# Kernel optimization log

Hardware: AMD Instinct MI355X
Metric: run time of the kernel (lower is better)

The kernel has to match this reference:

```python
import jax, jax.numpy as jnp
import numpy as np

T, A = 4096, 4          # tokens, atoms per token
N = T * A               # flat atoms
QB, KB = 32, 128        # query block / key window (AF3 atom transformer)
S = N // QB             # number of query subsets
H, DK = 4, 32           # heads, key dim per head
NB = 3                  # transformer blocks
CA, CP, CT = 128, 16, 384

# clipped sliding key window centered on each 32-atom query block
KIDX = jnp.clip(jnp.arange(S)[:, None] * QB - (KB - QB) // 2 + jnp.arange(KB)[None, :], 0, N - 1)

PARAM_SHAPES = [('w_ref_pos', (3, CA)), ('w_ref_mask', (1, CA)), ('w_ref_element', (CA, CA)), ('w_ref_charge', (1, CA)), ('w_ref_atom_name', (256, CA)), ('w_s2p_row', (CA, CP)), ('w_s2p_col', (CA, CP)), ('w_pair_offsets', (3, CP)), ('w_pair_dist', (1, CP)), ('w_pair_mask', (1, CP)), ('w_pair_mlp1', (CP, CP)), ('w_pair_mlp2', (CP, CP)), ('w_pair_mlp3', (CP, CP)), ('w_pair_ln', (CP,)), ('w_pair_logits', (CP, NB * H)), ('aq_lnw', (NB, CA)), ('aq_gw', (NB, CA, CA)), ('aq_gb', (NB, CA)), ('aq_sw', (NB, CA, CA)), ('ak_lnw', (NB, CA)), ('ak_gw', (NB, CA, CA)), ('ak_gb', (NB, CA)), ('ak_sw', (NB, CA, CA)), ('wq', (NB, CA, CA)), ('bq', (NB, CA)), ('wk', (NB, CA, CA)), ('wv', (NB, CA, CA)), ('wg', (NB, CA, CA)), ('azi_w', (NB, CA, CA)), ('azi_cw', (NB, CA, CA)), ('azi_cb', (NB, CA)), ('t_lnw', (NB, CA)), ('t_gw', (NB, CA, CA)), ('t_gb', (NB, CA)), ('t_sw', (NB, CA, CA)), ('glu1', (NB, CA, 2 * CA)), ('glu2', (NB, CA, 2 * CA)), ('t_azi_w', (NB, 2 * CA, CA)), ('t_azi_cw', (NB, CA, CA)), ('t_azi_cb', (NB, CA)), ('w_project', (CA, CT))]


def _ln(x, w=None, eps=1e-5):
    mu = jnp.mean(x, -1, keepdims=True)
    var = jnp.var(x, -1, keepdims=True)
    xn = (x - mu) * jax.lax.rsqrt(var + eps)
    return xn * w if w is not None else xn


def _ada_ln(x, cond, lnw, gw, gb, sw):
    c = _ln(cond, lnw)
    return jax.nn.sigmoid(c @ gw + gb) * _ln(x) + c @ sw


def setup_inputs() -> dict:
    ks = iter(jax.random.split(jax.random.key(0), 64))
    d = {}
    d['positions'] = jax.random.normal(next(ks), (T, A, 3), jnp.float32) * 3.0
    d['mask'] = jnp.ones((T, A), jnp.float32)
    d['element'] = jax.random.randint(next(ks), (T, A), 0, 128, jnp.int32)
    d['charge'] = jax.random.normal(next(ks), (T, A), jnp.float32)
    d['atom_name_chars'] = jax.random.randint(next(ks), (T, A, 4), 0, 64, jnp.int32)
    d['ref_space_uid'] = jax.random.randint(next(ks), (T, A), 0, T, jnp.int32)
    for nm, shp in PARAM_SHAPES:
        if nm.endswith('lnw') or nm == 'w_pair_ln':
            d[nm] = jnp.ones(shp, jnp.float32)
        else:
            d[nm] = jax.random.normal(next(ks), shp, jnp.float32) * 0.02
    return d


def _forward(positions, mask, charge, w_ref_pos, w_ref_mask, w_ref_element, w_ref_charge, w_ref_atom_name, w_s2p_row, w_s2p_col, w_pair_offsets, w_pair_dist, w_pair_mask, w_pair_mlp1, w_pair_mlp2, w_pair_mlp3, w_pair_ln, w_pair_logits, aq_lnw, aq_gw, aq_gb, aq_sw, ak_lnw, ak_gw, ak_gb, ak_sw, wq, bq, wk, wv, wg, azi_w, azi_cw, azi_cb, t_lnw, t_gw, t_gb, t_sw, glu1, glu2, t_azi_w, t_azi_cw, t_azi_cb, w_project, element, atom_name_chars, ref_space_uid):
    dt = positions.dtype
    pos = positions.reshape(N, 3)
    m = mask.reshape(N, 1)
    # per_atom_cond
    el1h = jax.nn.one_hot(element.reshape(N), 128, dtype=dt)
    nm1h = jax.nn.one_hot(atom_name_chars.reshape(N, 4), 64, dtype=dt).reshape(N, 256)
    ch = jnp.arcsinh(charge.reshape(N, 1))
    act = pos @ w_ref_pos + m @ w_ref_mask + el1h @ w_ref_element + ch @ w_ref_charge + nm1h @ w_ref_atom_name
    act = act * m
    qsc = act.reshape(S, QB, CA)  # queries_single_cond
    # pair conditioning
    uid = ref_space_uid.reshape(N)
    q_uid, k_uid = uid.reshape(S, QB), uid[KIDX]
    q_pos, k_pos = pos.reshape(S, QB, 3), pos[KIDX]
    valid = (q_uid[:, :, None] == k_uid[:, None, :]).astype(dt)[..., None]  # [S,QB,KB,1]
    off = q_pos[:, :, None, :] - k_pos[:, None, :, :]  # [S,QB,KB,3]
    pair = (off @ w_pair_offsets) * valid
    sq = jnp.sum(off * off, -1, keepdims=True)
    pair = pair + ((1.0 / (1.0 + sq)) @ w_pair_dist) * valid
    ksc = act[KIDX]  # keys_single_cond [S,KB,CA]
    pair = pair + (jax.nn.relu(qsc) @ w_s2p_row)[:, :, None, :] + (jax.nn.relu(ksc) @ w_s2p_col)[:, None, :, :]
    pair = pair + valid @ w_pair_mask
    t = jax.nn.relu(pair) @ w_pair_mlp1
    t = jax.nn.relu(t) @ w_pair_mlp2
    t = jax.nn.relu(t) @ w_pair_mlp3
    pair = pair + t
    # pair logits for all blocks: [NB, S, H, QB, KB]
    pl = (_ln(pair, w_pair_ln) @ w_pair_logits).reshape(S, QB, KB, NB, H)
    pl = jnp.transpose(pl, (3, 0, 4, 1, 2))
    qact = qsc
    scale = DK ** -0.5
    for i in range(NB):
        kact = qact.reshape(N, CA)[KIDX]
        xq = _ada_ln(qact, qsc, aq_lnw[i], aq_gw[i], aq_gb[i], aq_sw[i])
        xk = _ada_ln(kact, ksc, ak_lnw[i], ak_gw[i], ak_gb[i], ak_sw[i])
        q = (xq @ wq[i] + bq[i]).reshape(S, QB, H, DK)
        k = (xk @ wk[i]).reshape(S, KB, H, DK)
        logits = jnp.einsum('sqhd,skhd->shqk', q * scale, k) + pl[i]
        aw = jax.nn.softmax(logits, axis=-1)
        v = (xk @ wv[i]).reshape(S, KB, H, DK)
        o = jnp.einsum('shqk,skhd->sqhd', aw, v).reshape(S, QB, CA)
        o = o * jax.nn.sigmoid(xq @ wg[i])
        o = (o @ azi_w[i]) * jax.nn.sigmoid(qsc @ azi_cw[i] + azi_cb[i])  # AdaptiveZeroInit
        qact = qact + o
        xt = _ada_ln(qact, qsc, t_lnw[i], t_gw[i], t_gb[i], t_sw[i])
        xt = jax.nn.silu(xt @ glu1[i]) * (xt @ glu2[i])  # SwiGLU
        xt = (xt @ t_azi_w[i]) * jax.nn.sigmoid(qsc @ t_azi_cw[i] + t_azi_cb[i])
        qact = qact + xt
    tok = jax.nn.relu(qact.reshape(T, A, CA) @ w_project)
    mm = mask[..., None]
    token_act = jnp.sum(tok * mm, -2) / jnp.maximum(jnp.sum(mm, -2), 1e-10)
    return token_act, qact, qsc, pair


def reference(positions, mask, element, charge, atom_name_chars, ref_space_uid, w_ref_pos, w_ref_mask, w_ref_element, w_ref_charge, w_ref_atom_name, w_s2p_row, w_s2p_col, w_pair_offsets, w_pair_dist, w_pair_mask, w_pair_mlp1, w_pair_mlp2, w_pair_mlp3, w_pair_ln, w_pair_logits, aq_lnw, aq_gw, aq_gb, aq_sw, ak_lnw, ak_gw, ak_gb, ak_sw, wq, bq, wk, wv, wg, azi_w, azi_cw, azi_cb, t_lnw, t_gw, t_gb, t_sw, glu1, glu2, t_azi_w, t_azi_cw, t_azi_cb, w_project):
    return _forward(positions, mask, charge, w_ref_pos, w_ref_mask, w_ref_element, w_ref_charge, w_ref_atom_name, w_s2p_row, w_s2p_col, w_pair_offsets, w_pair_dist, w_pair_mask, w_pair_mlp1, w_pair_mlp2, w_pair_mlp3, w_pair_ln, w_pair_logits, aq_lnw, aq_gw, aq_gb, aq_sw, ak_lnw, ak_gw, ak_gb, ak_sw, wq, bq, wk, wv, wg, azi_w, azi_cw, azi_cb, t_lnw, t_gw, t_gb, t_sw, glu1, glu2, t_azi_w, t_azi_cw, t_azi_cb, w_project, element, atom_name_chars, ref_space_uid)
```

## Files before the change

kernel.cpp:

```cpp
#include <hip/hip_runtime.h>
#include <math.h>

#define TT 4096
#define AA 4
#define NN 16384
#define QBQ 32
#define KBK 128
#define SS 512
#define HH 4
#define DKD 32
#define CAC 128
#define CPC 16
#define CTC 384

#define EPI_PLAIN 0
#define EPI_SIG   1
#define EPI_RELU  3

typedef __attribute__((ext_vector_type(8))) short bf16x8;
typedef __attribute__((ext_vector_type(4))) short s16x4;
typedef __attribute__((ext_vector_type(4))) float f32x4;

__device__ __forceinline__ float sig_(float x) { return 1.0f / (1.0f + __expf(-x)); }
__device__ __forceinline__ short f2bf(float f) {
    unsigned u = __float_as_uint(f);
    unsigned r = (u + 0x7FFFu + ((u >> 16) & 1u)) >> 16;
    return (short)r;
}
__device__ __forceinline__ float b2f(short s) {
    return __uint_as_float(((unsigned)(unsigned short)s) << 16);
}

struct PEnt { const float* src; const float* rs; short* dst; int K; int NC; };
struct PTab { PEnt e[49]; };

__global__ __launch_bounds__(256) void k_prep(PTab tab)
{
    const PEnt e = tab.e[blockIdx.y];
    const int ntx = e.NC >> 5, nty = e.K >> 5, nt = ntx * nty;
    __shared__ float sm[32][33];
    const int lx = threadIdx.x & 31, ly = threadIdx.x >> 5;
    for (int t = blockIdx.x; t < nt; t += gridDim.x) {
        const int ty = t / ntx, tx = t - ty * ntx;
        #pragma unroll
        for (int j = 0; j < 4; ++j) {
            const int k = ty * 32 + ly + j * 8;
            const int n = tx * 32 + lx;
            float v = e.src[(size_t)k * e.NC + n];
            if (e.rs) v *= e.rs[k];
            sm[ly + j * 8][lx] = v;
        }
        __syncthreads();
        #pragma unroll
        for (int j = 0; j < 4; ++j) {
            const int n = tx * 32 + ly + j * 8;
            const int k = ty * 32 + lx;
            e.dst[(size_t)n * e.K + k] = f2bf(sm[lx][ly + j * 8]);
        }
        __syncthreads();
    }
}

__global__ __launch_bounds__(128) void k_atom_cond(
    const float* __restrict__ pos, const float* __restrict__ msk,
    const int* __restrict__ elem, const float* __restrict__ chg,
    const int* __restrict__ chars,
    const float* __restrict__ w_pos, const float* __restrict__ w_msk,
    const float* __restrict__ w_elem, const float* __restrict__ w_chg,
    const float* __restrict__ w_name,
    const float* __restrict__ w_row, const float* __restrict__ w_col,
    float* __restrict__ qsc, float* __restrict__ qact,
    short* __restrict__ qsc_bf, short* __restrict__ qn_bf,
    float* __restrict__ rq, float* __restrict__ rk)
{
    const int n = blockIdx.x, c = threadIdx.x;
    const float p0 = pos[n*3+0], p1 = pos[n*3+1], p2 = pos[n*3+2];
    const float m = msk[n];
    const int   el = elem[n];
    const float ach = asinhf(chg[n]);
    const int c0 = chars[n*4+0], c1 = chars[n*4+1], c2 = chars[n*4+2], c3 = chars[n*4+3];

    float a = p0*w_pos[c] + p1*w_pos[CAC+c] + p2*w_pos[2*CAC+c]
            + m*w_msk[c] + w_elem[el*CAC+c] + ach*w_chg[c]
            + w_name[(c0      )*CAC+c] + w_name[( 64+c1)*CAC+c]
            + w_name[(128+c2)*CAC+c] + w_name[(192+c3)*CAC+c];
    a *= m;

    const size_t base = (size_t)n*CAC + c;
    qsc[base] = a; qact[base] = a; qsc_bf[base] = f2bf(a);

    __shared__ float red[128];
    __shared__ float sh[128];
    red[c] = a; __syncthreads();
    for (int off = 64; off > 0; off >>= 1) { if (c < off) red[c] += red[c+off]; __syncthreads(); }
    const float mu = red[0] * (1.0f/128.0f);
    __syncthreads();
    const float d = a - mu;
    red[c] = d*d; __syncthreads();
    for (int off = 64; off > 0; off >>= 1) { if (c < off) red[c] += red[c+off]; __syncthreads(); }
    const float var = red[0] * (1.0f/128.0f);
    qn_bf[base] = f2bf(d * rsqrtf(var + 1e-5f));
    __syncthreads();
    sh[c] = fmaxf(a, 0.0f);
    __syncthreads();
    if (c < 32) {
        const float* w = (c < 16) ? w_row : w_col;
        const int cc = c & 15;
        float acc = 0.0f;
        #pragma unroll 8
        for (int r = 0; r < 128; ++r) acc += sh[r] * w[r*CPC + cc];
        if (c < 16) rq[(size_t)n*CPC + cc] = acc;
        else        rk[(size_t)n*CPC + cc] = acc;
    }
}

__global__ __launch_bounds__(256) void k_pair(
    const float* __restrict__ pos, const int* __restrict__ uid,
    const float* __restrict__ rq, const float* __restrict__ rk,
    const float* __restrict__ w_ofs, const float* __restrict__ w_dist,
    const float* __restrict__ w_pm,
    const float* __restrict__ mlp1, const float* __restrict__ mlp2,
    const float* __restrict__ mlp3,
    const float* __restrict__ wln, const float* __restrict__ wpl,
    float* __restrict__ pair, short* __restrict__ plb)
{
    __shared__ float sm1[256], sm2[256], sm3[256], sofs[48], sdist[16], smask[16];
    __shared__ float swln[16], swpl[192];
    const int tid = threadIdx.x;
    sm1[tid] = mlp1[tid]; sm2[tid] = mlp2[tid]; sm3[tid] = mlp3[tid];
    if (tid < 48) sofs[tid] = w_ofs[tid];
    if (tid < 16) { sdist[tid] = w_dist[tid]; smask[tid] = w_pm[tid]; swln[tid] = wln[tid]; }
    if (tid < 192) swpl[tid] = wpl[tid];
    __syncthreads();

    const int gid = blockIdx.x*256 + tid;
    const int s = gid >> 12;
    const int rem = gid & 4095;
    const int q = rem >> 7, kk = rem & 127;
    const int n = s*QBQ + q;
    int kidx = s*QBQ - 48 + kk; kidx = max(0, min(NN-1, kidx));

    const float v = (uid[n] == uid[kidx]) ? 1.0f : 0.0f;
    const float o0 = pos[n*3+0]-pos[kidx*3+0];
    const float o1 = pos[n*3+1]-pos[kidx*3+1];
    const float o2 = pos[n*3+2]-pos[kidx*3+2];
    const float sq = o0*o0 + o1*o1 + o2*o2;
    const float inv = 1.0f/(1.0f + sq);

    const float* rqp = rq + (size_t)n*CPC;
    const float* rkp = rk + (size_t)kidx*CPC;

    float p[16], t1[16], t2[16];
    #pragma unroll
    for (int j = 0; j < 16; ++j)
        p[j] = v*(o0*sofs[j] + o1*sofs[16+j] + o2*sofs[32+j] + inv*sdist[j] + smask[j])
             + rqp[j] + rkp[j];
    #pragma unroll
    for (int j = 0; j < 16; ++j) {
        float acc = 0.0f;
        #pragma unroll
        for (int r = 0; r < 16; ++r) acc += fmaxf(p[r], 0.0f) * sm1[r*16+j];
        t1[j] = acc;
    }
    #pragma unroll
    for (int j = 0; j < 16; ++j) {
        float acc = 0.0f;
        #pragma unroll
        for (int r = 0; r < 16; ++r) acc += fmaxf(t1[r], 0.0f) * sm2[r*16+j];
        t2[j] = acc;
    }
    #pragma unroll
    for (int j = 0; j < 16; ++j) {
        float acc = 0.0f;
        #pragma unroll
        for (int r = 0; r < 16; ++r) acc += fmaxf(t2[r], 0.0f) * sm3[r*16+j];
        t1[j] = p[j] + acc;
    }
    float* op = pair + (size_t)gid*CPC;
    #pragma unroll
    for (int j = 0; j < 4; ++j)
        *(float4*)(op + j*4) = make_float4(t1[j*4], t1[j*4+1], t1[j*4+2], t1[j*4+3]);

    float sm = 0.0f;
    #pragma unroll
    for (int j = 0; j < 16; ++j) sm += t1[j];
    const float mu = sm * (1.0f/16.0f);
    float vq = 0.0f;
    #pragma unroll
    for (int j = 0; j < 16; ++j) { const float dd = t1[j]-mu; vq += dd*dd; }
    const float rs = rsqrtf(vq*(1.0f/16.0f) + 1e-5f);
    float xn[16];
    #pragma unroll
    for (int j = 0; j < 16; ++j) xn[j] = (t1[j]-mu)*rs*swln[j];
    #pragma unroll
    for (int i = 0; i < 3; ++i) {
        #pragma unroll
        for (int h = 0; h < 4; ++h) {
            float acc = 0.0f;
            #pragma unroll
            for (int j = 0; j < 16; ++j) acc += xn[j] * swpl[j*12 + i*4 + h];
            plb[((((size_t)i*SS + s)*HH + h)*QBQ + q)*KBK + kk] = f2bf(acc);
        }
    }
}

__global__ __launch_bounds__(128) void k_rowln(const float* __restrict__ x, float* __restrict__ y)
{
    const int n = blockIdx.x, c = threadIdx.x;
    __shared__ float red[128];
    const float v = x[(size_t)n*CAC + c];
    red[c] = v; __syncthreads();
    for (int off = 64; off > 0; off >>= 1) { if (c < off) red[c] += red[c+off]; __syncthreads(); }
    const float mu = red[0] * (1.0f/128.0f);
    __syncthreads();
    const float d = v - mu;
    red[c] = d*d; __syncthreads();
    for (int off = 64; off > 0; off >>= 1) { if (c < off) red[c] += red[c+off]; __syncthreads(); }
    const float var = red[0] * (1.0f/128.0f);
    y[(size_t)n*CAC + c] = d * rsqrtf(var + 1e-5f);
}

struct MJob {
    const short* A; const short* Bt; const float* bias;
    float* outF; short* outB;
    int K; int ostride; int epi;
};
struct MJobs { MJob j[8]; };

__global__ __launch_bounds__(256) void k_mm(MJobs jobs)
{
    __shared__ short As[128*64];
    __shared__ short Bs[128*64];
    const MJob J = jobs.j[blockIdx.y];
    const int tid = threadIdx.x;
    const int wave = tid >> 6, lane = tid & 63;
    const int l15 = lane & 15, l4 = lane >> 4;
    const int row0 = blockIdx.x * 128;
    const int K = J.K;

    f32x4 acc[2][8];
    #pragma unroll
    for (int m = 0; m < 2; ++m)
        #pragma unroll
        for (int n = 0; n < 8; ++n) acc[m][n] = (f32x4){0.f,0.f,0.f,0.f};

    for (int k0 = 0; k0 < K; k0 += 64) {
        #pragma unroll
        for (int j = 0; j < 4; ++j) {
            const int u = tid + j*256;
            const int r = u >> 3, ug = u & 7;
            const bf16x8 av = *(const bf16x8*)(J.A + (size_t)(row0 + r)*K + k0 + ug*8);
            *(bf16x8*)&As[r*64 + ((ug ^ (r & 7)) * 8)] = av;
            const bf16x8 bv = *(const bf16x8*)(J.Bt + (size_t)r*K + k0 + ug*8);
            *(bf16x8*)&Bs[r*64 + ((ug ^ (r & 7)) * 8)] = bv;
        }
        __syncthreads();
        #pragma unroll
        for (int ks = 0; ks < 2; ++ks) {
            bf16x8 af[2], bfr[8];
            #pragma unroll
            for (int m = 0; m < 2; ++m) {
                const int r = wave*32 + m*16 + l15;
                af[m] = *(const bf16x8*)&As[r*64 + (((ks*4 + l4) ^ (r & 7)) * 8)];
            }
            #pragma unroll
            for (int n = 0; n < 8; ++n) {
                const int c = n*16 + l15;
                bfr[n] = *(const bf16x8*)&Bs[c*64 + (((ks*4 + l4) ^ (c & 7)) * 8)];
            }
            #pragma unroll
            for (int m = 0; m < 2; ++m)
                #pragma unroll
                for (int n = 0; n < 8; ++n)
                    acc[m][n] = __builtin_amdgcn_mfma_f32_16x16x32_bf16(af[m], bfr[n], acc[m][n], 0, 0, 0);
        }
        __syncthreads();
    }

    float bval[8];
    #pragma unroll
    for (int n = 0; n < 8; ++n) bval[n] = 0.0f;
    if (J.bias) {
        #pragma unroll
        for (int n = 0; n < 8; ++n) bval[n] = J.bias[n*16 + l15];
    }
    const int epi = J.epi;
    #pragma unroll
    for (int m = 0; m < 2; ++m) {
        #pragma unroll
        for (int n = 0; n < 8; ++n) {
            const int col = n*16 + l15;
            #pragma unroll
            for (int reg = 0; reg < 4; ++reg) {
                const int row = row0 + wave*32 + m*16 + l4*4 + reg;
                float v = acc[m][n][reg] + bval[n];
                if (epi == EPI_SIG)  v = sig_(v);
                if (epi == EPI_RELU) v = fmaxf(v, 0.0f);
                if (J.outB) J.outB[(size_t)row*J.ostride + col] = f2bf(v);
                else        J.outF[(size_t)row*J.ostride + col] = v;
            }
        }
    }
}

__global__ __launch_bounds__(512) void k_attn2(
    const float* __restrict__ qh, const float* __restrict__ kh,
    const float* __restrict__ vh, const short* __restrict__ pls,
    float* __restrict__ oh)
{
    __shared__ float sm_m[256], sm_l[256], sm_acc[256*17];
    const int s = blockIdx.x, tid = threadIdx.x;
    const int kh2 = tid >> 8;
    const int h = (tid >> 6) & 3;
    const int q = (tid >> 1) & 31;
    const int dh = tid & 1;
    const int n0 = s*QBQ;
    const int kbase = n0 - 48 + kh2*64;
    const float SCALE = 0.17677669529663687f;

    float qr[32];
    {
        const float* qp = qh + (size_t)(n0+q)*CAC + h*DKD;
        #pragma unroll
        for (int j = 0; j < 8; ++j) {
            const float4 v4 = *(const float4*)(qp + j*4);
            qr[j*4]=v4.x*SCALE; qr[j*4+1]=v4.y*SCALE; qr[j*4+2]=v4.z*SCALE; qr[j*4+3]=v4.w*SCALE;
        }
    }
    const short* plp = pls + (((size_t)s*HH + h)*QBQ + q)*KBK + kh2*64;

    float m = -1e30f, l = 0.0f;
    float acc[16];
    #pragma unroll
    for (int j = 0; j < 16; ++j) acc[j] = 0.0f;

    for (int kb4 = 0; kb4 < 16; ++kb4) {
        const s16x4 p4 = *(const s16x4*)(plp + kb4*4);
        float pv[4];
        #pragma unroll
        for (int j = 0; j < 4; ++j) pv[j] = b2f(p4[j]);
        #pragma unroll
        for (int j = 0; j < 4; ++j) {
            const int kb = kb4*4 + j;
            int kidx = kbase + kb; kidx = max(0, min(NN-1, kidx));
            const float* kp = kh + (size_t)kidx*CAC + h*DKD;
            float dot = 0.0f;
            #pragma unroll
            for (int jj = 0; jj < 8; ++jj) {
                const float4 kv = *(const float4*)(kp + jj*4);
                dot += qr[jj*4]*kv.x + qr[jj*4+1]*kv.y + qr[jj*4+2]*kv.z + qr[jj*4+3]*kv.w;
            }
            const float sv = dot + pv[j];
            if (sv > m) {
                const float corr = __expf(m - sv);
                l *= corr;
                #pragma unroll
                for (int d = 0; d < 16; ++d) acc[d] *= corr;
                m = sv;
            }
            const float w = __expf(sv - m);
            l += w;
            const float* vp = vh + (size_t)kidx*CAC + h*DKD + dh*16;
            #pragma unroll
            for (int jj = 0; jj < 4; ++jj) {
                const float4 vv = *(const float4*)(vp + jj*4);
                acc[jj*4]   = fmaf(w, vv.x, acc[jj*4]);
                acc[jj*4+1] = fmaf(w, vv.y, acc[jj*4+1]);
                acc[jj*4+2] = fmaf(w, vv.z, acc[jj*4+2]);
                acc[jj*4+3] = fmaf(w, vv.w, acc[jj*4+3]);
            }
        }
    }

    const int part = tid & 255;
    if (kh2 == 1) {
        sm_m[part] = m; sm_l[part] = l;
        #pragma unroll
        for (int j = 0; j < 16; ++j) sm_acc[part*17 + j] = acc[j];
    }
    __syncthreads();
    if (kh2 == 0) {
        const float m2 = sm_m[part], l2 = sm_l[part];
        const float mm = fmaxf(m, m2);
        const float c1 = __expf(m - mm), c2 = __expf(m2 - mm);
        const float inv = 1.0f / (l*c1 + l2*c2);
        float* op = oh + (size_t)(n0+q)*CAC + h*DKD + dh*16;
        #pragma unroll
        for (int jj = 0; jj < 4; ++jj) {
            float o0 = (acc[jj*4  ]*c1 + sm_acc[part*17+jj*4  ]*c2) * inv;
            float o1 = (acc[jj*4+1]*c1 + sm_acc[part*17+jj*4+1]*c2) * inv;
            float o2 = (acc[jj*4+2]*c1 + sm_acc[part*17+jj*4+2]*c2) * inv;
            float o3 = (acc[jj*4+3]*c1 + sm_acc[part*17+jj*4+3]*c2) * inv;
            *(float4*)op = make_float4(o0,o1,o2,o3);
            op += 4;
        }
    }
}

__global__ __launch_bounds__(256) void k_ada2(
    const float* __restrict__ qa,
    const short* __restrict__ G1, const short* __restrict__ S1,
    const short* __restrict__ G2, const short* __restrict__ S2,
    short* __restrict__ x1, short* __restrict__ x2)
{
    const int i = blockIdx.x*256 + threadIdx.x;
    const float4 a = ((const float4*)qa)[i];
    const s16x4 g1 = ((const s16x4*)G1)[i], s1 = ((const s16x4*)S1)[i];
    const s16x4 g2 = ((const s16x4*)G2)[i], s2 = ((const s16x4*)S2)[i];
    s16x4 o1, o2;
    o1[0] = f2bf(b2f(g1[0])*a.x + b2f(s1[0]));
    o1[1] = f2bf(b2f(g1[1])*a.y + b2f(s1[1]));
    o1[2] = f2bf(b2f(g1[2])*a.z + b2f(s1[2]));
    o1[3] = f2bf(b2f(g1[3])*a.w + b2f(s1[3]));
    o2[0] = f2bf(b2f(g2[0])*a.x + b2f(s2[0]));
    o2[1] = f2bf(b2f(g2[1])*a.y + b2f(s2[1]));
    o2[2] = f2bf(b2f(g2[2])*a.z + b2f(s2[2]));
    o2[3] = f2bf(b2f(g2[3])*a.w + b2f(s2[3]));
    ((s16x4*)x1)[i] = o1;
    ((s16x4*)x2)[i] = o2;
}

__global__ __launch_bounds__(256) void k_ada1(
    const float* __restrict__ qa,
    const short* __restrict__ G1, const short* __restrict__ S1,
    short* __restrict__ x1)
{
    const int i = blockIdx.x*256 + threadIdx.x;
    const float4 a = ((const float4*)qa)[i];
    const s16x4 g1 = ((const s16x4*)G1)[i], s1 = ((const s16x4*)S1)[i];
    s16x4 o1;
    o1[0] = f2bf(b2f(g1[0])*a.x + b2f(s1[0]));
    o1[1] = f2bf(b2f(g1[1])*a.y + b2f(s1[1]));
    o1[2] = f2bf(b2f(g1[2])*a.z + b2f(s1[2]));
    o1[3] = f2bf(b2f(g1[3])*a.w + b2f(s1[3]));
    ((s16x4*)x1)[i] = o1;
}

__global__ __launch_bounds__(256) void k_og(
    const float* __restrict__ o, const float* __restrict__ g, short* __restrict__ og)
{
    const int i = blockIdx.x*256 + threadIdx.x;
    const float4 a = ((const float4*)o)[i];
    const float4 b = ((const float4*)g)[i];
    s16x4 r;
    r[0] = f2bf(a.x*b.x); r[1] = f2bf(a.y*b.y); r[2] = f2bf(a.z*b.z); r[3] = f2bf(a.w*b.w);
    ((s16x4*)og)[i] = r;
}

__global__ __launch_bounds__(256) void k_axpy_g(
    float* __restrict__ y, const float* __restrict__ t,
    const short* __restrict__ g, short* __restrict__ ybf)
{
    const int i = blockIdx.x*256 + threadIdx.x;
    float4 yv = ((const float4*)y)[i];
    const float4 tv = ((const float4*)t)[i];
    const s16x4 gv = ((const s16x4*)g)[i];
    yv.x += tv.x * b2f(gv[0]);
    yv.y += tv.y * b2f(gv[1]);
    yv.z += tv.z * b2f(gv[2]);
    yv.w += tv.w * b2f(gv[3]);
    ((float4*)y)[i] = yv;
    if (ybf) {
        s16x4 r;
        r[0] = f2bf(yv.x); r[1] = f2bf(yv.y); r[2] = f2bf(yv.z); r[3] = f2bf(yv.w);
        ((s16x4*)ybf)[i] = r;
    }
}

__global__ __launch_bounds__(256) void k_silu_bf(
    const float* __restrict__ h1, const float* __restrict__ h2, short* __restrict__ hs)
{
    const int i = blockIdx.x*256 + threadIdx.x;
    const float4 a = ((const float4*)h1)[i];
    const float4 b = ((const float4*)h2)[i];
    s16x4 r;
    r[0] = f2bf(a.x * sig_(a.x) * b.x);
    r[1] = f2bf(a.y * sig_(a.y) * b.y);
    r[2] = f2bf(a.z * sig_(a.z) * b.z);
    r[3] = f2bf(a.w * sig_(a.w) * b.w);
    ((s16x4*)hs)[i] = r;
}

__global__ __launch_bounds__(256) void k_token_reduce(
    const float* __restrict__ tok, const float* __restrict__ msk, float* __restrict__ out)
{
    const int gid = blockIdx.x*256 + threadIdx.x;
    const int t = gid / CTC, c = gid - t*CTC;
    float num = 0.0f, den = 0.0f;
    #pragma unroll
    for (int a = 0; a < AA; ++a) {
        const float mv = msk[t*AA + a];
        num += tok[(size_t)(t*AA+a)*CTC + c] * mv;
        den += mv;
    }
    out[gid] = num / fmaxf(den, 1e-10f);
}

static inline MJob mj(const short* A, const short* Bt, const float* bias,
                      float* outF, short* outB, int K, int ostride, int epi)
{
    MJob j; j.A=A; j.Bt=Bt; j.bias=bias; j.outF=outF; j.outB=outB;
    j.K=K; j.ostride=ostride; j.epi=epi; return j;
}

extern "C" void kernel_launch(void* const* d_in, const int* in_sizes, int n_in,
                              void* d_out, int out_size, void* d_ws, size_t ws_size,
                              hipStream_t stream)
{
    const float* positions = (const float*)d_in[0];
    const float* maskp     = (const float*)d_in[1];
    const int*   element   = (const int*  )d_in[2];
    const float* charge    = (const float*)d_in[3];
    const int*   chars     = (const int*  )d_in[4];
    const int*   uid       = (const int*  )d_in[5];
    const float* w_ref_pos      = (const float*)d_in[6];
    const float* w_ref_mask     = (const float*)d_in[7];
    const float* w_ref_element  = (const float*)d_in[8];
    const float* w_ref_charge   = (const float*)d_in[9];
    const float* w_ref_atom_name= (const float*)d_in[10];
    const float* w_s2p_row      = (const float*)d_in[11];
    const float* w_s2p_col      = (const float*)d_in[12];
    const float* w_pair_offsets = (const float*)d_in[13];
    const float* w_pair_dist    = (const float*)d_in[14];
    const float* w_pair_mask    = (const float*)d_in[15];
    const float* w_pair_mlp1    = (const float*)d_in[16];
    const float* w_pair_mlp2    = (const float*)d_in[17];
    const float* w_pair_mlp3    = (const float*)d_in[18];
    const float* w_pair_ln      = (const float*)d_in[19];
    const float* w_pair_logits  = (const float*)d_in[20];
    const float* aq_lnw = (const float*)d_in[21];
    const float* aq_gw  = (const float*)d_in[22];
    const float* aq_gb  = (const float*)d_in[23];
    const float* aq_sw  = (const float*)d_in[24];
    const float* ak_lnw = (const float*)d_in[25];
    const float* ak_gw  = (const float*)d_in[26];
    const float* ak_gb  = (const float*)d_in[27];
    const float* ak_sw  = (const float*)d_in[28];
    const float* wq     = (const float*)d_in[29];
    const float* bq     = (const float*)d_in[30];
    const float* wk     = (const float*)d_in[31];
    const float* wv     = (const float*)d_in[32];
    const float* wg     = (const float*)d_in[33];
    const float* azi_w  = (const float*)d_in[34];
    const float* azi_cw = (const float*)d_in[35];
    const float* azi_cb = (const float*)d_in[36];
    const float* t_lnw  = (const float*)d_in[37];
    const float* t_gw   = (const float*)d_in[38];
    const float* t_gb   = (const float*)d_in[39];
    const float* t_sw   = (const float*)d_in[40];
    const float* glu1   = (const float*)d_in[41];
    const float* glu2   = (const float*)d_in[42];
    const float* t_azi_w  = (const float*)d_in[43];
    const float* t_azi_cw = (const float*)d_in[44];
    const float* t_azi_cb = (const float*)d_in[45];
    const float* w_project= (const float*)d_in[46];

    float* token_o = (float*)d_out;
    float* qact = token_o + 1572864;
    float* qsc  = token_o + 3670016;
    float* pair = token_o + 5767168;

    char* W = (char*)d_ws;
    short* pl_bf   = (short*)(W);
    short* wbf     = (short*)(W + 50331648);
    short* qn_bf   = (short*)(W + 52428800);
    short* qsc_bf  = (short*)(W + 56623104);
    float* qa      = (float*)(W + 60817408);
    short* Gq_bf   = (short*)(W + 69206016);
    short* Sq_bf   = (short*)(W + 73400320);
    short* Gk_bf   = (short*)(W + 77594624);
    short* Sk_bf   = (short*)(W + 81788928);
    short* Gt_bf   = (short*)(W + 85983232);
    short* St_bf   = (short*)(W + 90177536);
    short* Ag_bf   = (short*)(W + 94371840);
    short* Tg_bf   = (short*)(W + 98566144);
    short* xq_bf   = (short*)(W + 102760448);
    short* xk_bf   = (short*)(W + 106954752);
    float* w_q     = (float*)(W + 111149056);
    float* w_k     = (float*)(W + 119537664);
    float* w_v     = (float*)(W + 127926272);
    float* w_g     = (float*)(W + 136314880);
    float* w_o     = (float*)(W + 144703488);
    short* og_bf   = (short*)(W + 153092096);
    short* hs_bf   = (short*)(W + 157286400);
    short* qact_bf = (short*)(W + 165675008);
    float* rq      = (float*)(W + 169869312);
    float* rk      = (float*)(W + 174063616);
    float* h1  = w_q;
    float* h2  = w_v;
    float* tok = w_q;

    (void)in_sizes; (void)n_in; (void)out_size; (void)ws_size;

    const size_t LSTR = 311296;
    const size_t oGQ=0, oSQ=16384, oGK=32768, oSK=49152, oGT=65536, oST=81920,
                 oWQ=98304, oWK=114688, oWV=131072, oWG=147456, oAZ=163840,
                 oACW=180224, oTCW=196608, oG1=212992, oG2=245760, oTAW=278528;
    const size_t oPROJ = 3*LSTR;

    {
        PTab tab{};
        int e = 0;
        for (int i = 0; i < 3; ++i) {
            short* L = wbf + (size_t)i*LSTR;
            const size_t oM = (size_t)i*CAC*CAC, oV = (size_t)i*CAC, oGL = (size_t)i*CAC*2*CAC;
            tab.e[e++] = {aq_gw+oM,  aq_lnw+oV, L+oGQ,  128, 128};
            tab.e[e++] = {aq_sw+oM,  aq_lnw+oV, L+oSQ,  128, 128};
            tab.e[e++] = {ak_gw+oM,  ak_lnw+oV, L+oGK,  128, 128};
            tab.e[e++] = {ak_sw+oM,  ak_lnw+oV, L+oSK,  128, 128};
            tab.e[e++] = {t_gw+oM,   t_lnw+oV,  L+oGT,  128, 128};
            tab.e[e++] = {t_sw+oM,   t_lnw+oV,  L+oST,  128, 128};
            tab.e[e++] = {wq+oM,     nullptr,   L+oWQ,  128, 128};
            tab.e[e++] = {wk+oM,     nullptr,   L+oWK,  128, 128};
            tab.e[e++] = {wv+oM,     nullptr,   L+oWV,  128, 128};
            tab.e[e++] = {wg+oM,     nullptr,   L+oWG,  128, 128};
            tab.e[e++] = {azi_w+oM,  nullptr,   L+oAZ,  128, 128};
            tab.e[e++] = {azi_cw+oM, nullptr,   L+oACW, 128, 128};
            tab.e[e++] = {t_azi_cw+oM,nullptr,  L+oTCW, 128, 128};
            tab.e[e++] = {glu1+oGL,  nullptr,   L+oG1,  128, 256};
            tab.e[e++] = {glu2+oGL,  nullptr,   L+oG2,  128, 256};
            tab.e[e++] = {t_azi_w+oGL,nullptr,  L+oTAW, 256, 128};
        }
        tab.e[e++] = {w_project, nullptr, wbf+oPROJ, 128, 384};
        k_prep<<<dim3(48, 49), 256, 0, stream>>>(tab);
    }

    k_atom_cond<<<NN, 128, 0, stream>>>(positions, maskp, element, charge, chars,
        w_ref_pos, w_ref_mask, w_ref_element, w_ref_charge, w_ref_atom_name,
        w_s2p_row, w_s2p_col, qsc, qact, qsc_bf, qn_bf, rq, rk);

    k_pair<<<(SS*QBQ*KBK)/256, 256, 0, stream>>>(positions, uid, rq, rk,
        w_pair_offsets, w_pair_dist, w_pair_mask, w_pair_mlp1, w_pair_mlp2, w_pair_mlp3,
        w_pair_ln, w_pair_logits, pair, pl_bf);

    for (int i = 0; i < 3; ++i) {
        short* L = wbf + (size_t)i*LSTR;
        const size_t oV = (size_t)i*CAC;

        k_rowln<<<NN, 128, 0, stream>>>(qact, qa);

        {
            MJobs js{};
            js.j[0] = mj(qn_bf,  L+oGQ,  aq_gb+oV,    nullptr, Gq_bf, 128, 128, EPI_SIG);
            js.j[1] = mj(qn_bf,  L+oSQ,  nullptr,     nullptr, Sq_bf, 128, 128, EPI_PLAIN);
            js.j[2] = mj(qn_bf,  L+oGK,  ak_gb+oV,    nullptr, Gk_bf, 128, 128, EPI_SIG);
            js.j[3] = mj(qn_bf,  L+oSK,  nullptr,     nullptr, Sk_bf, 128, 128, EPI_PLAIN);
            js.j[4] = mj(qn_bf,  L+oGT,  t_gb+oV,     nullptr, Gt_bf, 128, 128, EPI_SIG);
            js.j[5] = mj(qn_bf,  L+oST,  nullptr,     nullptr, St_bf, 128, 128, EPI_PLAIN);
            js.j[6] = mj(qsc_bf, L+oACW, azi_cb+oV,   nullptr, Ag_bf, 128, 128, EPI_SIG);
            js.j[7] = mj(qsc_bf, L+oTCW, t_azi_cb+oV, nullptr, Tg_bf, 128, 128, EPI_SIG);
            k_mm<<<dim3(128, 8), 256, 0, stream>>>(js);
        }
        k_ada2<<<2048, 256, 0, stream>>>(qa, Gq_bf, Sq_bf, Gk_bf, Sk_bf, xq_bf, xk_bf);
        {
            MJobs js{};
            js.j[0] = mj(xq_bf, L+oWQ, bq+oV,   w_q, nullptr, 128, 128, EPI_PLAIN);
            js.j[1] = mj(xk_bf, L+oWK, nullptr, w_k, nullptr, 128, 128, EPI_PLAIN);
            js.j[2] = mj(xk_bf, L+oWV, nullptr, w_v, nullptr, 128, 128, EPI_PLAIN);
            js.j[3] = mj(xq_bf, L+oWG, nullptr, w_g, nullptr, 128, 128, EPI_SIG);
            k_mm<<<dim3(128, 4), 256, 0, stream>>>(js);
        }
        k_attn2<<<SS, 512, 0, stream>>>(w_q, w_k, w_v, pl_bf + (size_t)i*8388608, w_o);
        k_og<<<2048, 256, 0, stream>>>(w_o, w_g, og_bf);
        {
            MJobs js{};
            js.j[0] = mj(og_bf, L+oAZ, nullptr, w_o, nullptr, 128, 128, EPI_PLAIN);
            k_mm<<<dim3(128, 1), 256, 0, stream>>>(js);
        }
        k_axpy_g<<<2048, 256, 0, stream>>>(qact, w_o, Ag_bf, nullptr);
        k_rowln<<<NN, 128, 0, stream>>>(qact, qa);
        k_ada1<<<2048, 256, 0, stream>>>(qa, Gt_bf, St_bf, xq_bf);
        {
            MJobs js{};
            js.j[0] = mj(xq_bf, L+oG1,       nullptr, h1,     nullptr, 128, 256, EPI_PLAIN);
            js.j[1] = mj(xq_bf, L+oG1+16384, nullptr, h1+128, nullptr, 128, 256, EPI_PLAIN);
            js.j[2] = mj(xq_bf, L+oG2,       nullptr, h2,     nullptr, 128, 256, EPI_PLAIN);
            js.j[3] = mj(xq_bf, L+oG2+16384, nullptr, h2+128, nullptr, 128, 256, EPI_PLAIN);
            k_mm<<<dim3(128, 4), 256, 0, stream>>>(js);
        }
        k_silu_bf<<<4096, 256, 0, stream>>>(h1, h2, hs_bf);
        {
            MJobs js{};
            js.j[0] = mj(hs_bf, L+oTAW, nullptr, w_o, nullptr, 256, 128, EPI_PLAIN);
            k_mm<<<dim3(128, 1), 256, 0, stream>>>(js);
        }
        k_axpy_g<<<2048, 256, 0, stream>>>(qact, w_o, Tg_bf, (i == 2) ? qact_bf : nullptr);
    }

    {
        MJobs js{};
        js.j[0] = mj(qact_bf, wbf+oPROJ,       nullptr, tok,     nullptr, 128, 384, EPI_RELU);
        js.j[1] = mj(qact_bf, wbf+oPROJ+16384, nullptr, tok+128, nullptr, 128, 384, EPI_RELU);
        js.j[2] = mj(qact_bf, wbf+oPROJ+32768, nullptr, tok+256, nullptr, 128, 384, EPI_RELU);
        k_mm<<<dim3(128, 3), 256, 0, stream>>>(js);
    }
    k_token_reduce<<<(TT*CTC)/256, 256, 0, stream>>>(tok, maskp, token_o);
}
```

Before: 1.033 ms.

## Fuse residual, layernorm and adaLN; fold gating into GEMM A-load and SiLU-GLU epilogue

Merges the residual gated update, row layernorm and adaptive-LN modulation into a single per-row kernel, deferring the transition residual into the next block's first kernel with double-buffered gate buffers. The attention output gating is folded into the A-tile load of a dedicated GEMM, and the two GLU projections are computed in one GEMM with the SiLU-multiply in the epilogue. This removes several elementwise launches and the fp32 h1/h2 intermediates. The cost is more complex control flow and a GLU kernel that carries two accumulator sets.

```diff
diff --git a/kernel.cpp b/kernel.cpp
--- a/kernel.cpp
+++ b/kernel.cpp
@@ -204,20 +204,35 @@
     }
 }
 
-__global__ __launch_bounds__(128) void k_rowln(const float* __restrict__ x, float* __restrict__ y)
+__global__ __launch_bounds__(128) void k_resada(
+    float* __restrict__ qact, const float* __restrict__ o,
+    const short* __restrict__ g,
+    const short* __restrict__ G1, const short* __restrict__ S1,
+    const short* __restrict__ G2, const short* __restrict__ S2,
+    short* __restrict__ x1, short* __restrict__ x2, short* __restrict__ ybf)
 {
     const int n = blockIdx.x, c = threadIdx.x;
-    __shared__ float red[128];
-    const float v = x[(size_t)n*CAC + c];
-    red[c] = v; __syncthreads();
-    for (int off = 64; off > 0; off >>= 1) { if (c < off) red[c] += red[c+off]; __syncthreads(); }
-    const float mu = red[0] * (1.0f/128.0f);
-    __syncthreads();
-    const float d = v - mu;
-    red[c] = d*d; __syncthreads();
-    for (int off = 64; off > 0; off >>= 1) { if (c < off) red[c] += red[c+off]; __syncthreads(); }
-    const float var = red[0] * (1.0f/128.0f);
-    y[(size_t)n*CAC + c] = d * rsqrtf(var + 1e-5f);
+    const size_t base = (size_t)n*CAC + c;
+    float a = qact[base];
+    if (o) {
+        a += o[base] * b2f(g[base]);
+        qact[base] = a;
+    }
+    if (x1) {
+        __shared__ float red[128];
+        red[c] = a; __syncthreads();
+        for (int off = 64; off > 0; off >>= 1) { if (c < off) red[c] += red[c+off]; __syncthreads(); }
+        const float mu = red[0] * (1.0f/128.0f);
+        __syncthreads();
+        const float d = a - mu;
+        red[c] = d*d; __syncthreads();
+        for (int off = 64; off > 0; off >>= 1) { if (c < off) red[c] += red[c+off]; __syncthreads(); }
+        const float var = red[0] * (1.0f/128.0f);
+        const float ln = d * rsqrtf(var + 1e-5f);
+        x1[base] = f2bf(b2f(G1[base])*ln + b2f(S1[base]));
+        if (x2) x2[base] = f2bf(b2f(G2[base])*ln + b2f(S2[base]));
+    }
+    if (ybf) ybf[base] = f2bf(a);
 }
 
 struct MJob {
@@ -301,6 +316,156 @@
             }
         }
     }
+}
+
+__global__ __launch_bounds__(256) void k_mm_og(
+    const float* __restrict__ Ao, const float* __restrict__ Agt,
+    const short* __restrict__ Bt, float* __restrict__ out)
+{
+    __shared__ short As[128*64];
+    __shared__ short Bs[128*64];
+    const int tid = threadIdx.x;
+    const int wave = tid >> 6, lane = tid & 63;
+    const int l15 = lane & 15, l4 = lane >> 4;
+    const int row0 = blockIdx.x * 128;
+
+    f32x4 acc[2][8];
+    #pragma unroll
+    for (int m = 0; m < 2; ++m)
+        #pragma unroll
+        for (int n = 0; n < 8; ++n) acc[m][n] = (f32x4){0.f,0.f,0.f,0.f};
+
+    for (int k0 = 0; k0 < 128; k0 += 64) {
+        #pragma unroll
+        for (int j = 0; j < 4; ++j) {
+            const int u = tid + j*256;
+            const int r = u >> 3, ug = u & 7;
+            const size_t ab = (size_t)(row0 + r)*128 + k0 + ug*8;
+            const float4 oa = *(const float4*)(Ao + ab);
+            const float4 ob = *(const float4*)(Ao + ab + 4);
+            const float4 ga = *(const float4*)(Agt + ab);
+            const float4 gb = *(const float4*)(Agt + ab + 4);
+            bf16x8 av;
+            av[0]=f2bf(oa.x*ga.x); av[1]=f2bf(oa.y*ga.y); av[2]=f2bf(oa.z*ga.z); av[3]=f2bf(oa.w*ga.w);
+            av[4]=f2bf(ob.x*gb.x); av[5]=f2bf(ob.y*gb.y); av[6]=f2bf(ob.z*gb.z); av[7]=f2bf(ob.w*gb.w);
+            *(bf16x8*)&As[r*64 + ((ug ^ (r & 7)) * 8)] = av;
+            const bf16x8 bv = *(const bf16x8*)(Bt + (size_t)r*128 + k0 + ug*8);
+            *(bf16x8*)&Bs[r*64 + ((ug ^ (r & 7)) * 8)] = bv;
+        }
+        __syncthreads();
+        #pragma unroll
+        for (int ks = 0; ks < 2; ++ks) {
+            bf16x8 af[2], bfr[8];
+            #pragma unroll
+            for (int m = 0; m < 2; ++m) {
+                const int r = wave*32 + m*16 + l15;
+                af[m] = *(const bf16x8*)&As[r*64 + (((ks*4 + l4) ^ (r & 7)) * 8)];
+            }
+            #pragma unroll
+            for (int n = 0; n < 8; ++n) {
+                const int c = n*16 + l15;
+                bfr[n] = *(const bf16x8*)&Bs[c*64 + (((ks*4 + l4) ^ (c & 7)) * 8)];
+            }
+            #pragma unroll
+            for (int m = 0; m < 2; ++m)
+                #pragma unroll
+                for (int n = 0; n < 8; ++n)
+                    acc[m][n] = __builtin_amdgcn_mfma_f32_16x16x32_bf16(af[m], bfr[n], acc[m][n], 0, 0, 0);
+        }
+        __syncthreads();
+    }
+
+    #pragma unroll
+    for (int m = 0; m < 2; ++m)
+        #pragma unroll
+        for (int n = 0; n < 8; ++n) {
+            const int col = n*16 + l15;
+            #pragma unroll
+            for (int reg = 0; reg < 4; ++reg) {
+                const int row = row0 + wave*32 + m*16 + l4*4 + reg;
+                out[(size_t)row*128 + col] = acc[m][n][reg];
+            }
+        }
+}
+
+__global__ __launch_bounds__(256) void k_mm_glu(
+    const short* __restrict__ A, const short* __restrict__ B1t,
+    const short* __restrict__ B2t, short* __restrict__ out)
+{
+    __shared__ short As[128*64];
+    __shared__ short B1s[64*64];
+    __shared__ short B2s[64*64];
+    const int tid = threadIdx.x;
+    const int wave = tid >> 6, lane = tid & 63;
+    const int l15 = lane & 15, l4 = lane >> 4;
+    const int row0 = blockIdx.x * 128;
+    const int col0 = blockIdx.y * 64;
+
+    f32x4 acc1[2][4], acc2[2][4];
+    #pragma unroll
+    for (int m = 0; m < 2; ++m)
+        #pragma unroll
+        for (int n = 0; n < 4; ++n) {
+            acc1[m][n] = (f32x4){0.f,0.f,0.f,0.f};
+            acc2[m][n] = (f32x4){0.f,0.f,0.f,0.f};
+        }
+
+    for (int k0 = 0; k0 < 128; k0 += 64) {
+        #pragma unroll
+        for (int j = 0; j < 4; ++j) {
+            const int u = tid + j*256;
+            const int r = u >> 3, ug = u & 7;
+            const bf16x8 av = *(const bf16x8*)(A + (size_t)(row0 + r)*128 + k0 + ug*8);
+            *(bf16x8*)&As[r*64 + ((ug ^ (r & 7)) * 8)] = av;
+        }
+        #pragma unroll
+        for (int j = 0; j < 2; ++j) {
+            const int u = tid + j*256;
+            const int r = u >> 3, ug = u & 7;
+            const bf16x8 b1 = *(const bf16x8*)(B1t + (size_t)(col0 + r)*128 + k0 + ug*8);
+            *(bf16x8*)&B1s[r*64 + ((ug ^ (r & 7)) * 8)] = b1;
+            const bf16x8 b2 = *(const bf16x8*)(B2t + (size_t)(col0 + r)*128 + k0 + ug*8);
+            *(bf16x8*)&B2s[r*64 + ((ug ^ (r & 7)) * 8)] = b2;
+        }
+        __syncthreads();
+        #pragma unroll
+        for (int ks = 0; ks < 2; ++ks) {
+            bf16x8 af[2], bq1[4], bq2[4];
+            #pragma unroll
+            for (int m = 0; m < 2; ++m) {
+                const int r = wave*32 + m*16 + l15;
+                af[m] = *(const bf16x8*)&As[r*64 + (((ks*4 + l4) ^ (r & 7)) * 8)];
+            }
+            #pragma unroll
+            for (int n = 0; n < 4; ++n) {
+                const int c = n*16 + l15;
+                bq1[n] = *(const bf16x8*)&B1s[c*64 + (((ks*4 + l4) ^ (c & 7)) * 8)];
+                bq2[n] = *(const bf16x8*)&B2s[c*64 + (((ks*4 + l4) ^ (c & 7)) * 8)];
+            }
+            #pragma unroll
+            for (int m = 0; m < 2; ++m)
+                #pragma unroll
+                for (int n = 0; n < 4; ++n) {
+                    acc1[m][n] = __builtin_amdgcn_mfma_f32_16x16x32_bf16(af[m], bq1[n], acc1[m][n], 0, 0, 0);
+                    acc2[m][n] = __builtin_amdgcn_mfma_f32_16x16x32_bf16(af[m], bq2[n], acc2[m][n], 0, 0, 0);
+                }
+        }
+        __syncthreads();
+    }
+
+    #pragma unroll
+    for (int m = 0; m < 2; ++m)
+        #pragma unroll
+        for (int n = 0; n < 4; ++n) {
+            const int col = col0 + n*16 + l15;
+            #pragma unroll
+            for (int reg = 0; reg < 4; ++reg) {
+                const int row = row0 + wave*32 + m*16 + l4*4 + reg;
+                const float a1 = acc1[m][n][reg];
+                const float h = a1 * sig_(a1) * acc2[m][n][reg];
+                out[(size_t)row*256 + col] = f2bf(h);
+            }
+        }
 }
 
 __global__ __launch_bounds__(512) void k_attn2(
@@ -395,90 +560,6 @@
             op += 4;
         }
     }
-}
-
-__global__ __launch_bounds__(256) void k_ada2(
-    const float* __restrict__ qa,
-    const short* __restrict__ G1, const short* __restrict__ S1,
-    const short* __restrict__ G2, const short* __restrict__ S2,
-    short* __restrict__ x1, short* __restrict__ x2)
-{
-    const int i = blockIdx.x*256 + threadIdx.x;
-    const float4 a = ((const float4*)qa)[i];
-    const s16x4 g1 = ((const s16x4*)G1)[i], s1 = ((const s16x4*)S1)[i];
-    const s16x4 g2 = ((const s16x4*)G2)[i], s2 = ((const s16x4*)S2)[i];
-    s16x4 o1, o2;
-    o1[0] = f2bf(b2f(g1[0])*a.x + b2f(s1[0]));
-    o1[1] = f2bf(b2f(g1[1])*a.y + b2f(s1[1]));
-    o1[2] = f2bf(b2f(g1[2])*a.z + b2f(s1[2]));
-    o1[3] = f2bf(b2f(g1[3])*a.w + b2f(s1[3]));
-    o2[0] = f2bf(b2f(g2[0])*a.x + b2f(s2[0]));
-    o2[1] = f2bf(b2f(g2[1])*a.y + b2f(s2[1]));
-    o2[2] = f2bf(b2f(g2[2])*a.z + b2f(s2[2]));
-    o2[3] = f2bf(b2f(g2[3])*a.w + b2f(s2[3]));
-    ((s16x4*)x1)[i] = o1;
-    ((s16x4*)x2)[i] = o2;
-}
-
-__global__ __launch_bounds__(256) void k_ada1(
-    const float* __restrict__ qa,
-    const short* __restrict__ G1, const short* __restrict__ S1,
-    short* __restrict__ x1)
-{
-    const int i = blockIdx.x*256 + threadIdx.x;
-    const float4 a = ((const float4*)qa)[i];
-    const s16x4 g1 = ((const s16x4*)G1)[i], s1 = ((const s16x4*)S1)[i];
-    s16x4 o1;
-    o1[0] = f2bf(b2f(g1[0])*a.x + b2f(s1[0]));
-    o1[1] = f2bf(b2f(g1[1])*a.y + b2f(s1[1]));
-    o1[2] = f2bf(b2f(g1[2])*a.z + b2f(s1[2]));
-    o1[3] = f2bf(b2f(g1[3])*a.w + b2f(s1[3]));
-    ((s16x4*)x1)[i] = o1;
-}
-
-__global__ __launch_bounds__(256) void k_og(
-    const float* __restrict__ o, const float* __restrict__ g, short* __restrict__ og)
-{
-    const int i = blockIdx.x*256 + threadIdx.x;
-    const float4 a = ((const float4*)o)[i];
-    const float4 b = ((const float4*)g)[i];
-    s16x4 r;
-    r[0] = f2bf(a.x*b.x); r[1] = f2bf(a.y*b.y); r[2] = f2bf(a.z*b.z); r[3] = f2bf(a.w*b.w);
-    ((s16x4*)og)[i] = r;
-}
-
-__global__ __launch_bounds__(256) void k_axpy_g(
-    float* __restrict__ y, const float* __restrict__ t,
-    const short* __restrict__ g, short* __restrict__ ybf)
-{
-    const int i = blockIdx.x*256 + threadIdx.x;
-    float4 yv = ((const float4*)y)[i];
-    const float4 tv = ((const float4*)t)[i];
-    const s16x4 gv = ((const s16x4*)g)[i];
-    yv.x += tv.x * b2f(gv[0]);
-    yv.y += tv.y * b2f(gv[1]);
-    yv.z += tv.z * b2f(gv[2]);
-    yv.w += tv.w * b2f(gv[3]);
-    ((float4*)y)[i] = yv;
-    if (ybf) {
-        s16x4 r;
-        r[0] = f2bf(yv.x); r[1] = f2bf(yv.y); r[2] = f2bf(yv.z); r[3] = f2bf(yv.w);
-        ((s16x4*)ybf)[i] = r;
-    }
-}
-
-__global__ __launch_bounds__(256) void k_silu_bf(
-    const float* __restrict__ h1, const float* __restrict__ h2, short* __restrict__ hs)
-{
-    const int i = blockIdx.x*256 + threadIdx.x;
-    const float4 a = ((const float4*)h1)[i];
-    const float4 b = ((const float4*)h2)[i];
-    s16x4 r;
-    r[0] = f2bf(a.x * sig_(a.x) * b.x);
-    r[1] = f2bf(a.y * sig_(a.y) * b.y);
-    r[2] = f2bf(a.z * sig_(a.z) * b.z);
-    r[3] = f2bf(a.w * sig_(a.w) * b.w);
-    ((s16x4*)hs)[i] = r;
 }
 
 __global__ __launch_bounds__(256) void k_token_reduce(
@@ -565,7 +646,7 @@
     short* wbf     = (short*)(W + 50331648);
     short* qn_bf   = (short*)(W + 52428800);
     short* qsc_bf  = (short*)(W + 56623104);
-    float* qa      = (float*)(W + 60817408);
+    float* w_op    = (float*)(W + 60817408);
     short* Gq_bf   = (short*)(W + 69206016);
     short* Sq_bf   = (short*)(W + 73400320);
     short* Gk_bf   = (short*)(W + 77594624);
@@ -573,7 +654,7 @@
     short* Gt_bf   = (short*)(W + 85983232);
     short* St_bf   = (short*)(W + 90177536);
     short* Ag_bf   = (short*)(W + 94371840);
-    short* Tg_bf   = (short*)(W + 98566144);
+    short* Tg0_bf  = (short*)(W + 98566144);
     short* xq_bf   = (short*)(W + 102760448);
     short* xk_bf   = (short*)(W + 106954752);
     float* w_q     = (float*)(W + 111149056);
@@ -581,13 +662,11 @@
     float* w_v     = (float*)(W + 127926272);
     float* w_g     = (float*)(W + 136314880);
     float* w_o     = (float*)(W + 144703488);
-    short* og_bf   = (short*)(W + 153092096);
+    short* Tg1_bf  = (short*)(W + 153092096);
     short* hs_bf   = (short*)(W + 157286400);
     short* qact_bf = (short*)(W + 165675008);
     float* rq      = (float*)(W + 169869312);
     float* rk      = (float*)(W + 174063616);
-    float* h1  = w_q;
-    float* h2  = w_v;
     float* tok = w_q;
 
     (void)in_sizes; (void)n_in; (void)out_size; (void)ws_size;
@@ -636,8 +715,8 @@
     for (int i = 0; i < 3; ++i) {
         short* L = wbf + (size_t)i*LSTR;
         const size_t oV = (size_t)i*CAC;
-
-        k_rowln<<<NN, 128, 0, stream>>>(qact, qa);
+        short* Tg_cur  = (i & 1) ? Tg1_bf : Tg0_bf;
+        short* Tg_prev = (i & 1) ? Tg0_bf : Tg1_bf;
 
         {
             MJobs js{};
@@ -648,10 +727,12 @@
             js.j[4] = mj(qn_bf,  L+oGT,  t_gb+oV,     nullptr, Gt_bf, 128, 128, EPI_SIG);
             js.j[5] = mj(qn_bf,  L+oST,  nullptr,     nullptr, St_bf, 128, 128, EPI_PLAIN);
             js.j[6] = mj(qsc_bf, L+oACW, azi_cb+oV,   nullptr, Ag_bf, 128, 128, EPI_SIG);
-            js.j[7] = mj(qsc_bf, L+oTCW, t_azi_cb+oV, nullptr, Tg_bf, 128, 128, EPI_SIG);
+            js.j[7] = mj(qsc_bf, L+oTCW, t_azi_cb+oV, nullptr, Tg_cur, 128, 128, EPI_SIG);
             k_mm<<<dim3(128, 8), 256, 0, stream>>>(js);
         }
-        k_ada2<<<2048, 256, 0, stream>>>(qa, Gq_bf, Sq_bf, Gk_bf, Sk_bf, xq_bf, xk_bf);
+        k_resada<<<NN, 128, 0, stream>>>(qact,
+            (i > 0) ? w_op : nullptr, (i > 0) ? Tg_prev : nullptr,
+            Gq_bf, Sq_bf, Gk_bf, Sk_bf, xq_bf, xk_bf, nullptr);
         {
             MJobs js{};
             js.j[0] = mj(xq_bf, L+oWQ, bq+oV,   w_q, nullptr, 128, 128, EPI_PLAIN);
@@ -661,31 +742,18 @@
             k_mm<<<dim3(128, 4), 256, 0, stream>>>(js);
         }
         k_attn2<<<SS, 512, 0, stream>>>(w_q, w_k, w_v, pl_bf + (size_t)i*8388608, w_o);
-        k_og<<<2048, 256, 0, stream>>>(w_o, w_g, og_bf);
+        k_mm_og<<<dim3(128), 256, 0, stream>>>(w_o, w_g, L+oAZ, w_op);
+        k_resada<<<NN, 128, 0, stream>>>(qact, w_op, Ag_bf,
+            Gt_bf, St_bf, nullptr, nullptr, xq_bf, nullptr, nullptr);
+        k_mm_glu<<<dim3(128, 4), 256, 0, stream>>>(xq_bf, L+oG1, L+oG2, hs_bf);
         {
             MJobs js{};
-            js.j[0] = mj(og_bf, L+oAZ, nullptr, w_o, nullptr, 128, 128, EPI_PLAIN);
+            js.j[0] = mj(hs_bf, L+oTAW, nullptr, w_op, nullptr, 256, 128, EPI_PLAIN);
             k_mm<<<dim3(128, 1), 256, 0, stream>>>(js);
         }
-        k_axpy_g<<<2048, 256, 0, stream>>>(qact, w_o, Ag_bf, nullptr);
-        k_rowln<<<NN, 128, 0, stream>>>(qact, qa);
-        k_ada1<<<2048, 256, 0, stream>>>(qa, Gt_bf, St_bf, xq_bf);
-        {
-            MJobs js{};
-            js.j[0] = mj(xq_bf, L+oG1,       nullptr, h1,     nullptr, 128, 256, EPI_PLAIN);
-            js.j[1] = mj(xq_bf, L+oG1+16384, nullptr, h1+128, nullptr, 128, 256, EPI_PLAIN);
-            js.j[2] = mj(xq_bf, L+oG2,       nullptr, h2,     nullptr, 128, 256, EPI_PLAIN);
-            js.j[3] = mj(xq_bf, L+oG2+16384, nullptr, h2+128, nullptr, 128, 256, EPI_PLAIN);
-            k_mm<<<dim3(128, 4), 256, 0, stream>>>(js);
-        }
-        k_silu_bf<<<4096, 256, 0, stream>>>(h1, h2, hs_bf);
-        {
-            MJobs js{};
-            js.j[0] = mj(hs_bf, L+oTAW, nullptr, w_o, nullptr, 256, 128, EPI_PLAIN);
-            k_mm<<<dim3(128, 1), 256, 0, stream>>>(js);
-        }
-        k_axpy_g<<<2048, 256, 0, stream>>>(qact, w_o, Tg_bf, (i == 2) ? qact_bf : nullptr);
-    }
+    }
+    k_resada<<<NN, 128, 0, stream>>>(qact, w_op, Tg0_bf,
+        nullptr, nullptr, nullptr, nullptr, nullptr, nullptr, qact_bf);
 
     {
         MJobs js{};
```

Measured after the change: 943.6 us. 1.09x faster.
